# Kernel optimization log

Hardware: AMD Instinct MI355X
Metric: run time of the kernel (lower is better)

The kernel has to match this reference:

```python
import jax, jax.numpy as jnp
import numpy as np

D = 512
H = 8
DV = D // H  # 64
NEG_INF = -1e30


def setup_inputs() -> dict:
    key = jax.random.key(0)
    ks = jax.random.split(key, 10)
    B, S = 4, 2048
    x = jax.random.normal(ks[0], (B, D, S), dtype=jnp.float32)
    mask = jnp.ones((B, S), dtype=jnp.float32)
    s = 1.0 / np.sqrt(D)
    sv = 1.0 / np.sqrt(D)
    # per-head Linear(d -> dv) weights stacked: [H, dv, d] (torch Linear layout W @ x)
    Wq = jax.random.uniform(ks[1], (H, DV, D), jnp.float32, -s, s)
    bq = jax.random.uniform(ks[2], (H, DV), jnp.float32, -s, s)
    Wk = jax.random.uniform(ks[3], (H, DV, D), jnp.float32, -s, s)
    bk = jax.random.uniform(ks[4], (H, DV), jnp.float32, -s, s)
    Wv = jax.random.uniform(ks[5], (H, DV, D), jnp.float32, -s, s)
    bv = jax.random.uniform(ks[6], (H, DV), jnp.float32, -s, s)
    W0 = jax.random.uniform(ks[7], (D, D), jnp.float32, -sv, sv)
    b0 = jax.random.uniform(ks[8], (D,), jnp.float32, -sv, sv)
    return {"x": x, "mask": mask, "Wq": Wq, "bq": bq, "Wk": Wk, "bk": bk,
            "Wv": Wv, "bv": bv, "W0": W0, "b0": b0}


def reference(x, mask, Wq, bq, Wk, bk, Wv, bv, W0, b0):
    # x: [B, d, S] -> xt: [B, S, d]
    xt = jnp.transpose(x, (0, 2, 1))
    # fused per-head projections: [B, H, S, dv]
    q = jnp.einsum('bsd,hed->bhse', xt, Wq) + bq[None, :, None, :]
    k = jnp.einsum('bsd,hed->bhse', xt, Wk) + bk[None, :, None, :]
    v = jnp.einsum('bsd,hed->bhse', xt, Wv) + bv[None, :, None, :]
    dv = q.shape[-1]
    scores = jnp.einsum('bhse,bhte->bhst', q, k) * (1.0 / np.sqrt(dv))
    # mask_logits (QANet style): keep where mask==1, else -1e30; mask over key dim
    h_mask = mask[:, None, None, :]  # [B,1,1,S]
    scores = scores * h_mask + (1.0 - h_mask) * NEG_INF
    p = jax.nn.softmax(scores, axis=-1)
    # zero out fully-masked query rows via v_mask on query dim
    p = p * mask[:, None, :, None]
    out = jnp.einsum('bhst,bhte->bhse', p, v)  # [B,H,S,dv]
    # concat heads along feature dim -> [B, S, d]
    B, _, S, _ = out.shape
    heads = jnp.transpose(out, (0, 2, 1, 3)).reshape(B, S, -1)
    y = heads @ W0.T + b0  # output projection
    return jnp.transpose(y, (0, 2, 1))  # [B, d, S]
```

## Files before the change

### kernel.cpp

```cpp
#include <hip/hip_runtime.h>

#define B_  4
#define D_  512
#define H_  8
#define DV_ 64
#define S_  2048
#define LOG2E 1.442695041f

typedef __bf16 bf16;
typedef bf16  bf16x8 __attribute__((ext_vector_type(8)));
typedef bf16  bf16x4 __attribute__((ext_vector_type(4)));
typedef float f32x4  __attribute__((ext_vector_type(4)));

#define MFMA(a, b, c) __builtin_amdgcn_mfma_f32_16x16x32_bf16((a), (b), (c), 0, 0, 0)

#define GLOAD_LDS(g, l)                                                     \
    __builtin_amdgcn_global_load_lds(                                       \
        (const __attribute__((address_space(1))) void*)(g),                 \
        (__attribute__((address_space(3))) void*)(l), 16, 0, 0)

#define WAIT_VMCNT(n)                                                       \
    __builtin_amdgcn_s_waitcnt(((n) & 15) | (((n) >> 4) << 14) | (7 << 4) | (15 << 8))

__global__ __launch_bounds__(256) void prep(
    const float* __restrict__ x, const float* __restrict__ Wq,
    const float* __restrict__ Wk, const float* __restrict__ Wv,
    const float* __restrict__ W0, bf16* __restrict__ xb, bf16* __restrict__ Wb) {
    const int bid = blockIdx.x;
    if (bid < 1024) {
        __shared__ float tile[64][65];
        const int sblk = bid & 31;
        const int dblk = (bid >> 5) & 7;
        const int b    = bid >> 8;
        const int d0 = dblk * 64, s0 = sblk * 64;
        const int tx = threadIdx.x & 15;
        const int ty = threadIdx.x >> 4;
        const float* xp = x + (size_t)b * D_ * S_;
#pragma unroll
        for (int i = 0; i < 64; i += 16) {
            const float4 v = *(const float4*)&xp[(size_t)(d0 + ty + i) * S_ +
                                                 s0 + tx * 4];
            tile[tx * 4 + 0][ty + i] = v.x;
            tile[tx * 4 + 1][ty + i] = v.y;
            tile[tx * 4 + 2][ty + i] = v.z;
            tile[tx * 4 + 3][ty + i] = v.w;
        }
        __syncthreads();
        bf16* xbp = xb + ((size_t)b * S_ + s0) * D_ + d0;
        const int srow0 = threadIdx.x >> 3;
        const int d8    = (threadIdx.x & 7) * 8;
#pragma unroll
        for (int i = 0; i < 2; ++i) {
            const int srow = srow0 + i * 32;
            bf16x8 hv;
#pragma unroll
            for (int j = 0; j < 8; ++j) hv[j] = (bf16)tile[srow][d8 + j];
            *(bf16x8*)&xbp[(size_t)srow * D_ + d8] = hv;
        }
    } else {
        const int f0 = ((bid - 1024) * 256 + threadIdx.x) * 16;
        const int src = f0 >> 18;
        const int off = f0 & 262143;
        const float* W = (src == 0) ? Wq : (src == 1) ? Wk : (src == 2) ? Wv : W0;
        float4 v0 = *(const float4*)&W[off];
        float4 v1 = *(const float4*)&W[off + 4];
        float4 v2 = *(const float4*)&W[off + 8];
        float4 v3 = *(const float4*)&W[off + 12];
        bf16x8 h0 = {(bf16)v0.x, (bf16)v0.y, (bf16)v0.z, (bf16)v0.w,
                     (bf16)v1.x, (bf16)v1.y, (bf16)v1.z, (bf16)v1.w};
        bf16x8 h1 = {(bf16)v2.x, (bf16)v2.y, (bf16)v2.z, (bf16)v2.w,
                     (bf16)v3.x, (bf16)v3.y, (bf16)v3.z, (bf16)v3.w};
        *(bf16x8*)&Wb[f0]     = h0;
        *(bf16x8*)&Wb[f0 + 8] = h1;
    }
}

__global__ __launch_bounds__(512) void gemm_qkv(
    const bf16* __restrict__ A, const bf16* __restrict__ Wb,
    const float* __restrict__ bq, const float* __restrict__ bk,
    const float* __restrict__ bv,
    bf16* __restrict__ Q, bf16* __restrict__ K, bf16* __restrict__ Vt) {
    __shared__ union {
        struct { bf16 A[2][8192]; bf16 B[2][8192]; } s;
        bf16 T[128][132];
    } sm;

    const int tid = threadIdx.x;
    const int w = tid >> 6, lane = tid & 63;
    const int m16 = lane & 15, quad = lane >> 4;
    const int wr = w & 1, wc = w >> 1;

    const int bid  = (blockIdx.x & 7) * 96 + (blockIdx.x >> 3);
    const int nblk = bid % 12;
    const int mblk = bid / 12;
    const int m0 = mblk * 128, n0 = nblk * 128;

#define QKV_STAGE(BUF, K0)                                                   \
    {                                                                        \
        const int cb_ = (w & 3) * 4;                                         \
        _Pragma("unroll")                                                    \
        for (int i_ = 0; i_ < 4; ++i_) {                                     \
            const int c_  = cb_ + i_;                                        \
            const int mt_ = c_ >> 1, kk_ = c_ & 1;                           \
            const int row_ = mt_ * 16 + m16;                                 \
            const int col_ = (K0) + kk_ * 32 + quad * 8;                     \
            if (w < 4)                                                       \
                GLOAD_LDS(&A[(size_t)(m0 + row_) * D_ + col_],               \
                          &sm.s.A[BUF][(c_ * 64 + lane) * 8]);               \
            else                                                             \
                GLOAD_LDS(&Wb[(size_t)(n0 + row_) * D_ + col_],              \
                          &sm.s.B[BUF][(c_ * 64 + lane) * 8]);               \
        }                                                                    \
    }

    f32x4 acc[4][2];
#pragma unroll
    for (int i = 0; i < 4; ++i)
#pragma unroll
        for (int j = 0; j < 2; ++j) acc[i][j] = (f32x4){0.f, 0.f, 0.f, 0.f};

    QKV_STAGE(0, 0);
    __syncthreads();

    for (int t = 0; t < 8; ++t) {
        const int cur = t & 1;
        if (t < 7) QKV_STAGE(cur ^ 1, (t + 1) * 64);
#pragma unroll
        for (int kk = 0; kk < 2; ++kk) {
            bf16x8 af[4], bfv[2];
#pragma unroll
            for (int tt = 0; tt < 4; ++tt)
                af[tt]  = *(const bf16x8*)&sm.s.A[cur][
                    (((wr * 4 + tt) * 2 + kk) * 64 + lane) * 8];
#pragma unroll
            for (int nt = 0; nt < 2; ++nt)
                bfv[nt] = *(const bf16x8*)&sm.s.B[cur][
                    (((wc * 2 + nt) * 2 + kk) * 64 + lane) * 8];
#pragma unroll
            for (int mt = 0; mt < 4; ++mt)
#pragma unroll
                for (int nt = 0; nt < 2; ++nt)
                    acc[mt][nt] = MFMA(af[mt], bfv[nt], acc[mt][nt]);
        }
        __syncthreads();
    }
#undef QKV_STAGE

    const int proj = n0 >> 9;
    const float* bias = (proj == 0) ? bq : (proj == 1) ? bk : bv;

    if (proj == 2) {
#pragma unroll
        for (int mt = 0; mt < 4; ++mt)
#pragma unroll
            for (int nt = 0; nt < 2; ++nt) {
                const int nr = (n0 + wc * 32 + nt * 16 + m16) & 511;
                const int h = nr >> 6, e = nr & 63;
                const float bia = bias[nr];
                const int srow = m0 + wr * 64 + mt * 16 + quad * 4;
                const int b = srow >> 11, s = srow & 2047;
                const int s2 = (s & ~31) | (quad * 8 + (mt & 1) * 4);
                bf16x4 hv;
#pragma unroll
                for (int r = 0; r < 4; ++r) hv[r] = (bf16)(acc[mt][nt][r] + bia);
                *(bf16x4*)&Vt[(((size_t)b * H_ + h) * DV_ + e) * S_ + s2] = hv;
            }
    } else {
#pragma unroll
        for (int mt = 0; mt < 4; ++mt)
#pragma unroll
            for (int nt = 0; nt < 2; ++nt) {
                const int nloc = wc * 32 + nt * 16 + m16;
                const float bia = bias[(n0 + nloc) & 511];
#pragma unroll
                for (int r = 0; r < 4; ++r)
                    sm.T[wr * 64 + mt * 16 + quad * 4 + r][nloc] =
                        (bf16)(acc[mt][nt][r] + bia);
            }
        __syncthreads();
        const int rloc = tid >> 2, cb = (tid & 3) * 32;
        const int M = m0 + rloc, b = M >> 11, s = M & 2047;
        const int nrb = (n0 + cb) & 511;
        const int h = nrb >> 6, eo = nrb & 63;
        bf16* dst = ((proj == 0) ? Q : K) +
                    (((size_t)b * H_ + h) * S_ + s) * DV_ + eo;
#pragma unroll
        for (int u = 0; u < 4; ++u)
            *(bf16x8*)&dst[u * 8] = *(const bf16x8*)&sm.T[rloc][cb + u * 8];
    }
}

__global__ __launch_bounds__(256, 2) void flash_attn(
    const bf16* __restrict__ Q, const bf16* __restrict__ K, const bf16* __restrict__ Vt,
    const float* __restrict__ mask, bf16* __restrict__ heads) {
    __shared__ union {
        struct {
            bf16 Kl[2][4][2048];
            bf16 Vl[2][4][2048];
            float Ms[2048];
        } s;
        struct { float O[64][65]; float L[64]; } red;
    } sm;

    const int bid  = blockIdx.x;
    const int bidx = (bid & 7) * 128 + (bid >> 3);
    const int qblk = bidx & 31;
    const int h    = (bidx >> 5) & 7;
    const int b    = bidx >> 8;
    const int q0   = qblk * 64;

    const int tid = threadIdx.x;
    const int w = tid >> 6, lane = tid & 63;
    const int m16 = lane & 15, quad = lane >> 4;

    const bf16* Qp = Q  + ((size_t)b * H_ + h) * S_ * DV_;
    const bf16* Kp = K  + ((size_t)b * H_ + h) * S_ * DV_;
    const bf16* Vp = Vt + ((size_t)b * H_ + h) * DV_ * S_;
    const float* mp = mask + (size_t)b * S_;

    const int krow = lane >> 3;
    const int kcol = ((lane & 7) ^ krow) * 8;
    const int vrow = lane >> 2;
    const int vcol = ((lane & 3) ^ (vrow & 3)) * 8;

#pragma unroll
    for (int p = 0; p < 2; ++p) {
        const float4 mv = *(const float4*)&mp[(p * 256 + tid) * 4];
        f32x4 t = {mv.x * LOG2E, mv.y * LOG2E, mv.z * LOG2E, mv.w * LOG2E};
        *(f32x4*)&sm.s.Ms[(p * 256 + tid) * 4] = t;
    }

    bf16x8 qf[4][2];
#pragma unroll
    for (int qt = 0; qt < 4; ++qt)
#pragma unroll
        for (int kk = 0; kk < 2; ++kk) {
            bf16x8 v = *(const bf16x8*)&Qp[(size_t)(q0 + qt * 16 + m16) * DV_ +
                                           kk * 32 + quad * 8];
#pragma unroll
            for (int i = 0; i < 8; ++i) v[i] = (bf16)((float)v[i] * 0.125f);
            qf[qt][kk] = v;
        }

    bf16x8 ones;
#pragma unroll
    for (int i = 0; i < 8; ++i) ones[i] = (bf16)1.0f;

    f32x4 o[4][4];
    f32x4 lacc[4];
#pragma unroll
    for (int mt = 0; mt < 4; ++mt)
#pragma unroll
        for (int qt = 0; qt < 4; ++qt) o[mt][qt] = (f32x4){0.f, 0.f, 0.f, 0.f};
#pragma unroll
    for (int qt = 0; qt < 4; ++qt) lacc[qt] = (f32x4){0.f, 0.f, 0.f, 0.f};

    {
        const int tw = w * 32;
#pragma unroll
        for (int p = 0; p < 4; ++p)
            GLOAD_LDS(&Kp[(size_t)(tw + p * 8 + krow) * DV_ + kcol],
                      &sm.s.Kl[0][w][(p * 64 + lane) * 8]);
#pragma unroll
        for (int p = 0; p < 4; ++p)
            GLOAD_LDS(&Vp[(size_t)(p * 16 + vrow) * S_ + tw + vcol],
                      &sm.s.Vl[0][w][(p * 64 + lane) * 8]);
    }
    __syncthreads();

    for (int i = 0; i < 16; ++i) {
        const int tw = i * 128 + w * 32;
        if (i < 15) {
            const int twn = tw + 128;
            const int nb = (i + 1) & 1;
#pragma unroll
            for (int p = 0; p < 4; ++p)
                GLOAD_LDS(&Kp[(size_t)(twn + p * 8 + krow) * DV_ + kcol],
                          &sm.s.Kl[nb][w][(p * 64 + lane) * 8]);
#pragma unroll
            for (int p = 0; p < 4; ++p)
                GLOAD_LDS(&Vp[(size_t)(p * 16 + vrow) * S_ + twn + vcol],
                          &sm.s.Vl[nb][w][(p * 64 + lane) * 8]);
            WAIT_VMCNT(12);
        } else {
            WAIT_VMCNT(4);
        }
        __builtin_amdgcn_sched_barrier(0);
        const int buf = i & 1;

        bf16x8 kf[2][2];
#pragma unroll
        for (int tt = 0; tt < 2; ++tt)
#pragma unroll
            for (int kk = 0; kk < 2; ++kk)
                kf[tt][kk] = *(const bf16x8*)&sm.s.Kl[buf][w][
                    ((tt * 16 + m16) * 8 + ((kk * 4 + quad) ^ (m16 & 7))) * 8];
        const f32x4 m2a = *(const f32x4*)&sm.s.Ms[tw + quad * 4];
        const f32x4 m2b = *(const f32x4*)&sm.s.Ms[tw + 16 + quad * 4];

        f32x4 sc[2][4];
#pragma unroll
        for (int tt = 0; tt < 2; ++tt)
#pragma unroll
            for (int qt = 0; qt < 4; ++qt) sc[tt][qt] = (f32x4){0.f, 0.f, 0.f, 0.f};
#pragma unroll
        for (int kk = 0; kk < 2; ++kk)
#pragma unroll
            for (int tt = 0; tt < 2; ++tt)
#pragma unroll
                for (int qt = 0; qt < 4; ++qt)
                    sc[tt][qt] = MFMA(kf[tt][kk], qf[qt][kk], sc[tt][qt]);

        f32x4 ngA, ngB;
#pragma unroll
        for (int r = 0; r < 4; ++r) {
            ngA[r] = (m2a[r] - LOG2E) * 8e29f;
            ngB[r] = (m2b[r] - LOG2E) * 8e29f;
        }
        bf16x8 pf[4];
#pragma unroll
        for (int qt = 0; qt < 4; ++qt)
#pragma unroll
            for (int r = 0; r < 4; ++r) {
                pf[qt][r]     = (bf16)__builtin_amdgcn_exp2f(
                    __builtin_fmaf(sc[0][qt][r], m2a[r], ngA[r]));
                pf[qt][4 + r] = (bf16)__builtin_amdgcn_exp2f(
                    __builtin_fmaf(sc[1][qt][r], m2b[r], ngB[r]));
            }

#pragma unroll
        for (int qt = 0; qt < 4; ++qt) lacc[qt] = MFMA(ones, pf[qt], lacc[qt]);

        if (i < 15) WAIT_VMCNT(8);
        else        WAIT_VMCNT(0);
        __builtin_amdgcn_sched_barrier(0);

        bf16x8 vf[4];
#pragma unroll
        for (int mt = 0; mt < 4; ++mt)
            vf[mt] = *(const bf16x8*)&sm.s.Vl[buf][w][
                ((mt * 16 + m16) * 4 + (quad ^ (m16 & 3))) * 8];

#pragma unroll
        for (int mt = 0; mt < 4; ++mt)
#pragma unroll
            for (int qt = 0; qt < 4; ++qt) o[mt][qt] = MFMA(vf[mt], pf[qt], o[mt][qt]);
    }

    __syncthreads();
#pragma unroll
    for (int ww = 0; ww < 4; ++ww) {
        if (w == ww) {
#pragma unroll
            for (int mt = 0; mt < 4; ++mt)
#pragma unroll
                for (int qt = 0; qt < 4; ++qt)
#pragma unroll
                    for (int r = 0; r < 4; ++r) {
                        float* slot = &sm.red.O[mt * 16 + quad * 4 + r][qt * 16 + m16];
                        *slot = (ww == 0) ? o[mt][qt][r] : (*slot + o[mt][qt][r]);
                    }
            if (quad == 0)
#pragma unroll
                for (int qt = 0; qt < 4; ++qt) {
                    float* ls = &sm.red.L[qt * 16 + m16];
                    *ls = (ww == 0) ? lacc[qt][0] : (*ls + lacc[qt][0]);
                }
        }
        __syncthreads();
    }

    const int ql = tid >> 2, ec = (tid & 3) * 16;
    const float l  = sm.red.L[ql];
    const float qm = mp[q0 + ql];
    const float inv = qm / l;
    bf16x8 hv[2];
#pragma unroll
    for (int c = 0; c < 2; ++c)
#pragma unroll
        for (int i = 0; i < 8; ++i)
            hv[c][i] = (bf16)(sm.red.O[ec + c * 8 + i][ql] * inv);
    bf16* dst = &heads[((size_t)b * S_ + q0 + ql) * D_ + h * DV_ + ec];
    *(bf16x8*)(dst)     = hv[0];
    *(bf16x8*)(dst + 8) = hv[1];
}

__global__ __launch_bounds__(512) void gemm_out(
    const bf16* __restrict__ A, const bf16* __restrict__ Wb,
    const float* __restrict__ b0, float* __restrict__ outp) {
    __shared__ bf16 Asl[2][8192];
    __shared__ bf16 Bsl[2][8192];

    const int tid = threadIdx.x;
    const int w = tid >> 6, lane = tid & 63;
    const int m16 = lane & 15, quad = lane >> 4;
    const int wr = w & 1, wc = w >> 1;

    const int bid  = (blockIdx.x & 7) * 32 + (blockIdx.x >> 3);
    const int nblk = bid & 3;
    const int mblk = bid >> 2;
    const int m0 = mblk * 128, n0 = nblk * 128;

#define OUT_STAGE(BUF, K0)                                                   \
    {                                                                        \
        const int cb_ = (w & 3) * 4;                                         \
        _Pragma("unroll")                                                    \
        for (int i_ = 0; i_ < 4; ++i_) {                                     \
            const int c_  = cb_ + i_;                                        \
            const int mt_ = c_ >> 1, kk_ = c_ & 1;                           \
            const int row_ = mt_ * 16 + m16;                                 \
            const int col_ = (K0) + kk_ * 32 + quad * 8;                     \
            if (w < 4)                                                       \
                GLOAD_LDS(&A[(size_t)(m0 + row_) * D_ + col_],               \
                          &Asl[BUF][(c_ * 64 + lane) * 8]);                  \
            else                                                             \
                GLOAD_LDS(&Wb[(size_t)(1536 + n0 + row_) * D_ + col_],       \
                          &Bsl[BUF][(c_ * 64 + lane) * 8]);                  \
        }                                                                    \
    }

    f32x4 acc[4][2];
#pragma unroll
    for (int i = 0; i < 4; ++i)
#pragma unroll
        for (int j = 0; j < 2; ++j) acc[i][j] = (f32x4){0.f, 0.f, 0.f, 0.f};

    OUT_STAGE(0, 0);
    __syncthreads();

    for (int t = 0; t < 8; ++t) {
        const int cur = t & 1;
        if (t < 7) OUT_STAGE(cur ^ 1, (t + 1) * 64);
#pragma unroll
        for (int kk = 0; kk < 2; ++kk) {
            bf16x8 af[4], bfv[2];
#pragma unroll
            for (int tt = 0; tt < 4; ++tt)
                af[tt]  = *(const bf16x8*)&Asl[cur][
                    (((wr * 4 + tt) * 2 + kk) * 64 + lane) * 8];
#pragma unroll
            for (int nt = 0; nt < 2; ++nt)
                bfv[nt] = *(const bf16x8*)&Bsl[cur][
                    (((wc * 2 + nt) * 2 + kk) * 64 + lane) * 8];
#pragma unroll
            for (int mt = 0; mt < 4; ++mt)
#pragma unroll
                for (int nt = 0; nt < 2; ++nt)
                    acc[mt][nt] = MFMA(af[mt], bfv[nt], acc[mt][nt]);
        }
        __syncthreads();
    }
#undef OUT_STAGE

#pragma unroll
    for (int mt = 0; mt < 4; ++mt)
#pragma unroll
        for (int nt = 0; nt < 2; ++nt) {
            const int n = n0 + wc * 32 + nt * 16 + m16;
            const float bia = b0[n];
            const int srow = m0 + wr * 64 + mt * 16 + quad * 4;
            const int b = srow >> 11, s = srow & 2047;
            float4 vv;
            vv.x = acc[mt][nt][0] + bia;
            vv.y = acc[mt][nt][1] + bia;
            vv.z = acc[mt][nt][2] + bia;
            vv.w = acc[mt][nt][3] + bia;
            *(float4*)&outp[((size_t)b * D_ + n) * S_ + s] = vv;
        }
}

extern "C" void kernel_launch(void* const* d_in, const int* in_sizes, int n_in,
                              void* d_out, int out_size, void* d_ws, size_t ws_size,
                              hipStream_t stream) {
    const float* x    = (const float*)d_in[0];
    const float* mask = (const float*)d_in[1];
    const float* Wq   = (const float*)d_in[2];
    const float* bq   = (const float*)d_in[3];
    const float* Wk   = (const float*)d_in[4];
    const float* bk   = (const float*)d_in[5];
    const float* Wv   = (const float*)d_in[6];
    const float* bv   = (const float*)d_in[7];
    const float* W0   = (const float*)d_in[8];
    const float* b0   = (const float*)d_in[9];
    float* out = (float*)d_out;

    char* ws = (char*)d_ws;
    const size_t SEG = (size_t)B_ * S_ * D_ * sizeof(bf16);
    bf16* xb    = (bf16*)(ws);
    bf16* Qb    = (bf16*)(ws + SEG);
    bf16* Kb    = (bf16*)(ws + 2 * SEG);
    bf16* Vt    = (bf16*)(ws + 3 * SEG);
    bf16* Wb    = (bf16*)(ws + 4 * SEG);
    bf16* heads = xb;

    prep<<<dim3(1024 + 256), dim3(256), 0, stream>>>(x, Wq, Wk, Wv, W0, xb, Wb);
    gemm_qkv<<<dim3(64 * 12), dim3(512), 0, stream>>>(xb, Wb, bq, bk, bv, Qb, Kb, Vt);
    flash_attn<<<dim3(B_ * H_ * (S_ / 64)), dim3(256), 0, stream>>>(Qb, Kb, Vt, mask, heads);
    gemm_out<<<dim3(64 * 4), dim3(512), 0, stream>>>(heads, Wb, b0, out);
}
```

Measured before the change: 191.0 us.

## Single-buffer V, pack mask into bits, raise flash_attn occupancy to 3

```diff
diff --git a/kernel.cpp b/kernel.cpp
--- a/kernel.cpp
+++ b/kernel.cpp
@@ -190,14 +190,14 @@
     }
 }
 
-__global__ __launch_bounds__(256, 2) void flash_attn(
+__global__ __launch_bounds__(256, 3) void flash_attn(
     const bf16* __restrict__ Q, const bf16* __restrict__ K, const bf16* __restrict__ Vt,
     const float* __restrict__ mask, bf16* __restrict__ heads) {
     __shared__ union {
         struct {
             bf16 Kl[2][4][2048];
-            bf16 Vl[2][4][2048];
-            float Ms[2048];
+            bf16 Vl[4][2048];
+            unsigned int Mb[64];
         } s;
         struct { float O[64][65]; float L[64]; } red;
     } sm;
@@ -223,11 +223,15 @@
     const int vrow = lane >> 2;
     const int vcol = ((lane & 3) ^ (vrow & 3)) * 8;
 
-#pragma unroll
-    for (int p = 0; p < 2; ++p) {
-        const float4 mv = *(const float4*)&mp[(p * 256 + tid) * 4];
-        f32x4 t = {mv.x * LOG2E, mv.y * LOG2E, mv.z * LOG2E, mv.w * LOG2E};
-        *(f32x4*)&sm.s.Ms[(p * 256 + tid) * 4] = t;
+    {
+        const float4 ma = *(const float4*)&mp[tid * 8];
+        const float4 mb2 = *(const float4*)&mp[tid * 8 + 4];
+        unsigned int byt =
+            (ma.x  != 0.f ?   1u : 0u) | (ma.y  != 0.f ?   2u : 0u) |
+            (ma.z  != 0.f ?   4u : 0u) | (ma.w  != 0.f ?   8u : 0u) |
+            (mb2.x != 0.f ?  16u : 0u) | (mb2.y != 0.f ?  32u : 0u) |
+            (mb2.z != 0.f ?  64u : 0u) | (mb2.w != 0.f ? 128u : 0u);
+        ((unsigned char*)sm.s.Mb)[tid] = (unsigned char)byt;
     }
 
     bf16x8 qf[4][2];
@@ -264,7 +268,7 @@
 #pragma unroll
         for (int p = 0; p < 4; ++p)
             GLOAD_LDS(&Vp[(size_t)(p * 16 + vrow) * S_ + tw + vcol],
-                      &sm.s.Vl[0][w][(p * 64 + lane) * 8]);
+                      &sm.s.Vl[w][(p * 64 + lane) * 8]);
     }
     __syncthreads();
 
@@ -277,11 +281,7 @@
             for (int p = 0; p < 4; ++p)
                 GLOAD_LDS(&Kp[(size_t)(twn + p * 8 + krow) * DV_ + kcol],
                           &sm.s.Kl[nb][w][(p * 64 + lane) * 8]);
-#pragma unroll
-            for (int p = 0; p < 4; ++p)
-                GLOAD_LDS(&Vp[(size_t)(p * 16 + vrow) * S_ + twn + vcol],
-                          &sm.s.Vl[nb][w][(p * 64 + lane) * 8]);
-            WAIT_VMCNT(12);
+            WAIT_VMCNT(8);
         } else {
             WAIT_VMCNT(4);
         }
@@ -295,8 +295,7 @@
             for (int kk = 0; kk < 2; ++kk)
                 kf[tt][kk] = *(const bf16x8*)&sm.s.Kl[buf][w][
                     ((tt * 16 + m16) * 8 + ((kk * 4 + quad) ^ (m16 & 7))) * 8];
-        const f32x4 m2a = *(const f32x4*)&sm.s.Ms[tw + quad * 4];
-        const f32x4 m2b = *(const f32x4*)&sm.s.Ms[tw + 16 + quad * 4];
+        const unsigned int mw = sm.s.Mb[tw >> 5];
 
         f32x4 sc[2][4];
 #pragma unroll
@@ -311,40 +310,45 @@
                 for (int qt = 0; qt < 4; ++qt)
                     sc[tt][qt] = MFMA(kf[tt][kk], qf[qt][kk], sc[tt][qt]);
 
-        f32x4 ngA, ngB;
-#pragma unroll
-        for (int r = 0; r < 4; ++r) {
-            ngA[r] = (m2a[r] - LOG2E) * 8e29f;
-            ngB[r] = (m2b[r] - LOG2E) * 8e29f;
-        }
+        const unsigned int nA = mw >> (quad * 4);
+        const unsigned int nB = mw >> (16 + quad * 4);
         bf16x8 pf[4];
 #pragma unroll
         for (int qt = 0; qt < 4; ++qt)
 #pragma unroll
             for (int r = 0; r < 4; ++r) {
-                pf[qt][r]     = (bf16)__builtin_amdgcn_exp2f(
-                    __builtin_fmaf(sc[0][qt][r], m2a[r], ngA[r]));
-                pf[qt][4 + r] = (bf16)__builtin_amdgcn_exp2f(
-                    __builtin_fmaf(sc[1][qt][r], m2b[r], ngB[r]));
+                const float eA = __builtin_amdgcn_exp2f(sc[0][qt][r] * LOG2E);
+                const float eB = __builtin_amdgcn_exp2f(sc[1][qt][r] * LOG2E);
+                pf[qt][r]     = ((nA >> r) & 1) ? (bf16)eA : (bf16)0.0f;
+                pf[qt][4 + r] = ((nB >> r) & 1) ? (bf16)eB : (bf16)0.0f;
             }
 
 #pragma unroll
         for (int qt = 0; qt < 4; ++qt) lacc[qt] = MFMA(ones, pf[qt], lacc[qt]);
 
-        if (i < 15) WAIT_VMCNT(8);
+        if (i < 15) WAIT_VMCNT(4);
         else        WAIT_VMCNT(0);
         __builtin_amdgcn_sched_barrier(0);
 
         bf16x8 vf[4];
 #pragma unroll
         for (int mt = 0; mt < 4; ++mt)
-            vf[mt] = *(const bf16x8*)&sm.s.Vl[buf][w][
+            vf[mt] = *(const bf16x8*)&sm.s.Vl[w][
                 ((mt * 16 + m16) * 4 + (quad ^ (m16 & 3))) * 8];
 
 #pragma unroll
         for (int mt = 0; mt < 4; ++mt)
 #pragma unroll
             for (int qt = 0; qt < 4; ++qt) o[mt][qt] = MFMA(vf[mt], pf[qt], o[mt][qt]);
+
+        __builtin_amdgcn_sched_barrier(0);
+        if (i < 15) {
+            const int twn = tw + 128;
+#pragma unroll
+            for (int p = 0; p < 4; ++p)
+                GLOAD_LDS(&Vp[(size_t)(p * 16 + vrow) * S_ + twn + vcol],
+                          &sm.s.Vl[w][(p * 64 + lane) * 8]);
+        }
     }
 
     __syncthreads();
```

After: 221.5 us. 1.16x slower.
